# Kernel optimization log

Measured on AMD Instinct MI355X. Metric: run time of the kernel, lower is better.

## Reference

```python
import jax, jax.numpy as jnp
import numpy as np

B, S, D = 4, 2048, 512
H, KD, VD = 8, 64, 64


def glorot(key, shape):
    fan_in, fan_out = shape[-2], shape[-1]
    limit = np.sqrt(6.0 / (fan_in + fan_out)).astype(np.float32)
    return jax.random.uniform(key, shape, jnp.float32, -limit, limit)


def setup_inputs() -> dict:
    key = jax.random.key(0)
    ks = jax.random.split(key, 6)
    input_tensor = jax.random.normal(ks[0], (B, S, D), jnp.float32)
    input_mask = jnp.ones((B, S), jnp.float32)
    # Per-head projections stacked along a leading head axis [H, D, kd/vd]
    Wq = glorot(ks[1], (H, D, KD))
    Wk = glorot(ks[2], (H, D, KD))
    Wv = glorot(ks[3], (H, D, VD))
    Wo = glorot(ks[4], (H * VD, VD))
    # dot_product_scales initialized to 1 in the original (tf.Variable(1))
    scales = jnp.ones((H,), jnp.float32)
    return {"input_tensor": input_tensor, "input_mask": input_mask,
            "Wq": Wq, "Wk": Wk, "Wv": Wv, "Wo": Wo, "scales": scales}


def reference(input_tensor, input_mask, Wq, Wk, Wv, Wo, scales):
    # Vectorized over the original per-head Python loop (identical math).
    q = jnp.einsum('bsd,hdk->bhsk', input_tensor, Wq)
    k = jnp.einsum('bsd,hdk->bhsk', input_tensor, Wk)
    v = jnp.einsum('bsd,hdv->bhsv', input_tensor, Wv)
    # dotproduct notation 'bik,bjk->bij' per head, scaled by per-head scale
    scores = jnp.einsum('bhik,bhjk->bhij', q, k) * scales[None, :, None, None]
    # reshape to [..., -1] then softmax == softmax over last (key) axis here
    attn = jax.nn.softmax(scores, axis=-1)
    # kv notation 'bij,bjv,bi,bj->biv' with the mask applied twice
    ctx = jnp.einsum('bhij,bhjv,bi,bj->bhiv', attn, v, input_mask, input_mask)
    # concat heads along last axis (head-major order, as in the loop)
    ctx = jnp.transpose(ctx, (0, 2, 1, 3)).reshape(ctx.shape[0], ctx.shape[2], -1)
    return ctx @ Wo
```

## Files before the change

kernel.cpp:

```cpp
#include <hip/hip_runtime.h>
#include <hip/hip_bf16.h>


typedef _Float16 f16x8 __attribute__((ext_vector_type(8)));
typedef float    f32x4  __attribute__((ext_vector_type(4)));
typedef float    f32x16 __attribute__((ext_vector_type(16)));

#define BB 4
#define SS 2048
#define DD 512
#define HH 8
#define KDIM 64

#define EXP2F(x) __builtin_amdgcn_exp2f(x)

#define GLOAD_LDS16(gp, lp)                                                   \
  __builtin_amdgcn_global_load_lds(                                          \
      (const __attribute__((address_space(1))) void*)(gp),                    \
      (__attribute__((address_space(3))) void*)(lp), 16, 0, 0)

#define SWZ(row, bc) ((row) * 128 + ((bc) ^ (((row) & 7) << 4)))

static __device__ __forceinline__ unsigned pk2(float a, float b) {
  auto h = __builtin_amdgcn_cvt_pkrtz(a, b);
  return __builtin_bit_cast(unsigned, h);
}

union PU { unsigned u[4]; f16x8 v; };

__global__ __launch_bounds__(256) void convert_x(
    const float* __restrict__ x, _Float16* __restrict__ xf) {
  size_t i = ((size_t)blockIdx.x * 256 + threadIdx.x) * 8;
  float4 a = *(const float4*)&x[i];
  float4 b = *(const float4*)&x[i + 4];
  float vv[8] = {a.x, a.y, a.z, a.w, b.x, b.y, b.z, b.w};
  _Float16 hb[8];
#pragma unroll
  for (int u = 0; u < 8; ++u) hb[u] = (_Float16)vv[u];
  *(uint4*)&xf[i] = *(uint4*)hb;
}

__global__ __launch_bounds__(256) void convert_w(
    const float* __restrict__ Wq, const float* __restrict__ Wk,
    const float* __restrict__ Wv, _Float16* __restrict__ wtf) {
  __shared__ float s_tile[64][65];
  const int t = threadIdx.x;
  const int kb = blockIdx.x;
  const int hw = blockIdx.y;
  const int which = hw >> 3, h = hw & 7;
  const float* W = (which == 0) ? Wq : (which == 1) ? Wk : Wv;
  const float* src = W + (size_t)h * DD * KDIM + (size_t)kb * 64 * KDIM;

  {
    int kk = t >> 2, c0 = (t & 3) * 16;
#pragma unroll
    for (int u = 0; u < 4; ++u)
      *(float4*)&s_tile[kk][c0 + u * 4] = *(const float4*)&src[kk * KDIM + c0 + u * 4];
  }
  __syncthreads();

  int kd = t >> 2, kk0 = (t & 3) * 16;
  int n = which * 512 + h * 64 + kd;
  _Float16 hb[16];
#pragma unroll
  for (int u = 0; u < 16; ++u) hb[u] = (_Float16)s_tile[kk0 + u][kd];
  size_t off = (size_t)n * DD + kb * 64 + kk0;
  *(uint4*)&wtf[off] = *(uint4*)&hb[0];
  *(uint4*)&wtf[off + 8] = *(uint4*)&hb[8];
}

__global__ __launch_bounds__(256) void convert_wo(
    const float* __restrict__ Wo, _Float16* __restrict__ woT) {
  __shared__ float s_tile[64][65];
  const int t = threadIdx.x;
  const int kb = blockIdx.x;
  const float* src = Wo + (size_t)kb * 64 * 64;
  {
    int kk = t >> 2, c0 = (t & 3) * 16;
#pragma unroll
    for (int u = 0; u < 4; ++u)
      *(float4*)&s_tile[kk][c0 + u * 4] = *(const float4*)&src[kk * 64 + c0 + u * 4];
  }
  __syncthreads();
  int col = t >> 2, kk0 = (t & 3) * 16;
  _Float16 hb[16];
#pragma unroll
  for (int u = 0; u < 16; ++u) hb[u] = (_Float16)s_tile[kk0 + u][col];
  size_t off = (size_t)col * DD + kb * 64 + kk0;
  *(uint4*)&woT[off] = *(uint4*)&hb[0];
  *(uint4*)&woT[off + 8] = *(uint4*)&hb[8];
}

__global__ __launch_bounds__(256) void qkv_gemm(
    const _Float16* __restrict__ xf, const _Float16* __restrict__ wtf,
    const float* __restrict__ mask, const float* __restrict__ scales,
    _Float16* __restrict__ qf, _Float16* __restrict__ kf,
    _Float16* __restrict__ vT) {
  __shared__ _Float16 Af[128 * 32], Bf[128 * 32];
  const int t = threadIdx.x, l = t & 63, w = t >> 6;
  const int wr = w >> 1, wc = w & 1;
  const int m0 = blockIdx.y * 128, n0 = blockIdx.x * 128;

  f32x4 acc[4][4];
#pragma unroll
  for (int m = 0; m < 4; ++m)
#pragma unroll
    for (int n = 0; n < 4; ++n) acc[m][n] = f32x4{0.f, 0.f, 0.f, 0.f};

  const int rl = l >> 2, ce = (l & 3) * 8;

  for (int kt = 0; kt < 16; ++kt) {
    const int k0 = kt * 32;
    __syncthreads();
#pragma unroll
    for (int i = 0; i < 2; ++i) {
      const int row = w * 32 + i * 16;
      const size_t aoff = (size_t)(m0 + row + rl) * DD + k0 + ce;
      const size_t boff = (size_t)(n0 + row + rl) * DD + k0 + ce;
      GLOAD_LDS16(xf + aoff, &Af[row * 32]);
      GLOAD_LDS16(wtf + boff, &Bf[row * 32]);
    }
    __syncthreads();

    f16x8 ah[4], bh[4];
#pragma unroll
    for (int m = 0; m < 4; ++m) {
      int r = wr * 64 + m * 16 + (l & 15);
      ah[m] = *(const f16x8*)&Af[r * 32 + (l >> 4) * 8];
    }
#pragma unroll
    for (int n = 0; n < 4; ++n) {
      int r = wc * 64 + n * 16 + (l & 15);
      bh[n] = *(const f16x8*)&Bf[r * 32 + (l >> 4) * 8];
    }
#pragma unroll
    for (int m = 0; m < 4; ++m)
#pragma unroll
      for (int n = 0; n < 4; ++n)
        acc[m][n] = __builtin_amdgcn_mfma_f32_16x16x32_f16(ah[m], bh[n], acc[m][n], 0, 0, 0);
  }

#pragma unroll
  for (int n = 0; n < 4; ++n) {
    int colg = n0 + wc * 64 + n * 16 + (l & 15);
    int which = colg >> 9, rem = colg & 511;
    int h = rem >> 6, kd = rem & 63;
    float qsc = (which == 0) ? scales[h] * 1.44269504f : 1.f;
#pragma unroll
    for (int m = 0; m < 4; ++m) {
      int row0 = m0 + wr * 64 + m * 16 + (l >> 4) * 4;
      if (which == 2) {
        int b = row0 >> 11, s0 = row0 & 2047;
        _Float16 tmp[4] __attribute__((aligned(8)));
#pragma unroll
        for (int j = 0; j < 4; ++j)
          tmp[j] = (_Float16)(acc[m][n][j] * mask[row0 + j]);
        *(uint2*)&vT[((size_t)(b * HH + h) * KDIM + kd) * SS + s0] = *(uint2*)tmp;
      } else {
        _Float16* dst = (which == 0) ? qf : kf;
#pragma unroll
        for (int j = 0; j < 4; ++j) {
          int row = row0 + j;
          int b = row >> 11, s = row & 2047;
          dst[(((size_t)b * HH + h) * SS + s) * KDIM + kd] =
              (_Float16)(acc[m][n][j] * qsc);
        }
      }
    }
  }
}

__global__ __launch_bounds__(256) void attn_kernel(
    const _Float16* __restrict__ qg, const _Float16* __restrict__ kg,
    const _Float16* __restrict__ vTg, const float* __restrict__ mask,
    _Float16* __restrict__ ctxf) {
  const int t = threadIdx.x;
  const int l = t & 63, w = t >> 6;
  const int lr = l & 31, hi = l >> 5;
  const int bh = blockIdx.y, b = bh >> 3, h = bh & 7;
  const int q0 = blockIdx.x * 128;

  __shared__ _Float16 ksf[64 * 64];
  __shared__ _Float16 vts[64 * 64];

  const size_t base = (size_t)bh * SS * KDIM;
  const size_t vbase = (size_t)bh * KDIM * SS;

  f16x8 qfr[4];
  const int s_q = q0 + w * 32 + lr;
#pragma unroll
  for (int kb = 0; kb < 4; ++kb)
    qfr[kb] = *(const f16x8*)&qg[base + (size_t)s_q * KDIM + kb * 16 + hi * 8];

  float m_s = -1e30f, lsum = 0.f;
  f32x16 oacc[2] = {};

  for (int kt = 0; kt < SS / 64; ++kt) {
    __syncthreads();
#pragma unroll
    for (int c = 0; c < 2; ++c) {
      const int r = w * 16 + c * 8 + (l >> 3);
      const int ecol = ((l & 7) * 8) ^ (((l >> 3) & 7) * 8);
      size_t koff = base + (size_t)(kt * 64 + r) * KDIM + ecol;
      size_t voff = vbase + (size_t)r * SS + kt * 64 + ecol;
      GLOAD_LDS16(kg + koff, ksf + (w * 16 + c * 8) * 64);
      GLOAD_LDS16(vTg + voff, vts + (w * 16 + c * 8) * 64);
    }
    __syncthreads();

    f32x16 st2[2];
#pragma unroll
    for (int jb = 0; jb < 2; ++jb) {
      f32x16 acc = {};
      const int krow = jb * 32 + lr;
#pragma unroll
      for (int kb = 0; kb < 4; ++kb) {
        f16x8 kfr = *(const f16x8*)((const char*)ksf + SWZ(krow, kb * 32 + hi * 16));
        acc = __builtin_amdgcn_mfma_f32_32x32x16_f16(kfr, qfr[kb], acc, 0, 0, 0);
      }
      st2[jb] = acc;
    }

    float mt = -1e30f;
#pragma unroll
    for (int jb = 0; jb < 2; ++jb)
#pragma unroll
      for (int rr = 0; rr < 16; ++rr) mt = fmaxf(mt, st2[jb][rr]);
    mt = fmaxf(mt, __shfl_xor(mt, 32, 64));

    if (!__all(mt <= m_s + 11.5f)) {
      float mn = fmaxf(m_s, mt);
      float rs = EXP2F(m_s - mn);
      m_s = mn;
      lsum *= rs;
#pragma unroll
      for (int nb = 0; nb < 2; ++nb)
#pragma unroll
        for (int rr = 0; rr < 16; ++rr) oacc[nb][rr] *= rs;
    }

    float psum = 0.f;
    unsigned wds[2][4][2];
#pragma unroll
    for (int jb = 0; jb < 2; ++jb)
#pragma unroll
      for (int g = 0; g < 4; ++g) {
        float p0 = EXP2F(st2[jb][g * 4 + 0] - m_s);
        float p1 = EXP2F(st2[jb][g * 4 + 1] - m_s);
        float p2 = EXP2F(st2[jb][g * 4 + 2] - m_s);
        float p3 = EXP2F(st2[jb][g * 4 + 3] - m_s);
        psum += (p0 + p1) + (p2 + p3);
        wds[jb][g][0] = pk2(p0, p1);
        wds[jb][g][1] = pk2(p2, p3);
      }
    psum += __shfl_xor(psum, 32, 64);
    lsum += psum;

#pragma unroll
    for (int kb = 0; kb < 4; ++kb) {
      const int jb = kb >> 1, gb = (kb & 1) * 2;
      unsigned ow0 = hi ? wds[jb][gb + 1][0] : wds[jb][gb][0];
      unsigned ow1 = hi ? wds[jb][gb + 1][1] : wds[jb][gb][1];
      unsigned sw0 = hi ? wds[jb][gb][0] : wds[jb][gb + 1][0];
      unsigned sw1 = hi ? wds[jb][gb][1] : wds[jb][gb + 1][1];
      unsigned r0 = (unsigned)__shfl_xor((int)sw0, 32, 64);
      unsigned r1 = (unsigned)__shfl_xor((int)sw1, 32, 64);
      PU pu;
      pu.u[0] = hi ? r0 : ow0;
      pu.u[1] = hi ? r1 : ow1;
      pu.u[2] = hi ? ow0 : r0;
      pu.u[3] = hi ? ow1 : r1;
#pragma unroll
      for (int nb = 0; nb < 2; ++nb) {
        f16x8 vf = *(const f16x8*)((const char*)vts + SWZ(nb * 32 + lr, kb * 32 + hi * 16));
        oacc[nb] = __builtin_amdgcn_mfma_f32_32x32x16_f16(vf, pu.v, oacc[nb], 0, 0, 0);
      }
    }
  }

  const float inv = mask[b * SS + s_q] / lsum;
  _Float16* dst = ctxf + ((size_t)b * SS + s_q) * (HH * KDIM) + h * KDIM;
#pragma unroll
  for (int nb = 0; nb < 2; ++nb)
#pragma unroll
    for (int g = 0; g < 4; ++g) {
      uint2 o;
      o.x = pk2(oacc[nb][g * 4 + 0] * inv, oacc[nb][g * 4 + 1] * inv);
      o.y = pk2(oacc[nb][g * 4 + 2] * inv, oacc[nb][g * 4 + 3] * inv);
      *(uint2*)&dst[nb * 32 + g * 8 + hi * 4] = o;
    }
}

__global__ __launch_bounds__(256) void oproj_gemm(
    const _Float16* __restrict__ ctxf, const _Float16* __restrict__ woT,
    float* __restrict__ out) {
  __shared__ _Float16 Af[64 * 32], Bf[64 * 32];
  const int t = threadIdx.x, l = t & 63, w = t >> 6;
  const int lr = l & 31, hi = l >> 5;
  const int wr = w >> 1, wc = w & 1;
  const size_t rowbase = (size_t)blockIdx.x * 64;
  const int rl = l >> 2, ce = (l & 3) * 8;

  f32x16 acc = {};
  for (int kt = 0; kt < 16; ++kt) {
    const int k0 = kt * 32;
    __syncthreads();
    {
      const int row = w * 16;
      GLOAD_LDS16(ctxf + (rowbase + row + rl) * DD + k0 + ce, &Af[row * 32]);
      GLOAD_LDS16(woT + (size_t)(row + rl) * DD + k0 + ce, &Bf[row * 32]);
    }
    __syncthreads();
#pragma unroll
    for (int ks = 0; ks < 2; ++ks) {
      f16x8 af = *(const f16x8*)&Af[(wr * 32 + lr) * 32 + ks * 16 + hi * 8];
      f16x8 bf = *(const f16x8*)&Bf[(wc * 32 + lr) * 32 + ks * 16 + hi * 8];
      acc = __builtin_amdgcn_mfma_f32_32x32x16_f16(af, bf, acc, 0, 0, 0);
    }
  }
#pragma unroll
  for (int rr = 0; rr < 16; ++rr) {
    int m = (rr & 3) + 8 * (rr >> 2) + 4 * hi;
    out[(rowbase + wr * 32 + m) * 64 + wc * 32 + lr] = acc[rr];
  }
}

extern "C" void kernel_launch(void* const* d_in, const int* in_sizes, int n_in,
                              void* d_out, int out_size, void* d_ws, size_t ws_size,
                              hipStream_t stream) {
  const float* x     = (const float*)d_in[0];
  const float* mask  = (const float*)d_in[1];
  const float* Wq    = (const float*)d_in[2];
  const float* Wk    = (const float*)d_in[3];
  const float* Wv    = (const float*)d_in[4];
  const float* Wo    = (const float*)d_in[5];
  const float* scales= (const float*)d_in[6];
  float* out = (float*)d_out;

  char* ws = (char*)d_ws;
  const size_t xb = (size_t)BB * SS * DD * sizeof(_Float16);
  const size_t wb = (size_t)3 * 512 * DD * sizeof(_Float16);
  const size_t wob = (size_t)64 * DD * sizeof(_Float16);
  const size_t qb = (size_t)BB * HH * SS * KDIM * sizeof(_Float16);

  _Float16* xfb = (_Float16*)(ws);
  _Float16* wtfb = (_Float16*)(ws + xb);
  _Float16* woTb = (_Float16*)(ws + xb + wb);
  char* p = ws + xb + wb + wob;
  _Float16* qfb = (_Float16*)(p);
  _Float16* kfb = (_Float16*)(p + qb);
  _Float16* vTb = (_Float16*)(p + 2 * qb);
  _Float16* ctxf = (_Float16*)(p + 3 * qb);

  convert_x<<<2048, 256, 0, stream>>>(x, xfb);
  convert_w<<<dim3(8, 24), 256, 0, stream>>>(Wq, Wk, Wv, wtfb);
  convert_wo<<<8, 256, 0, stream>>>(Wo, woTb);
  qkv_gemm<<<dim3(12, 64), 256, 0, stream>>>(xfb, wtfb, mask, scales,
                                             qfb, kfb, vTb);
  attn_kernel<<<dim3(SS / 128, BB * HH), 256, 0, stream>>>(qfb, kfb, vTb, mask, ctxf);
  oproj_gemm<<<128, 256, 0, stream>>>(ctxf, woTb, out);
}
```

Baseline: 115.2 us.

## Split attention over key dimension with a log-sum-exp combine kernel

Splits the attention key loop into four chunks across a new grid dimension. Each block writes a normalized partial output in fp16 plus its log-sum-exp, and a new combine kernel merges the partials and applies the mask. This raises the block count from 512 to 2048 to fill the GPU's CUs, at the cost of extra partial-output traffic, fp16 rounding of the partials, and one more launch. It also tree-reduces the row max, sums probabilities with fdot2 on the packed fp16 values, and simplifies the lane-swap selects.

```diff
diff --git a/kernel.cpp b/kernel.cpp
--- a/kernel.cpp
+++ b/kernel.cpp
@@ -5,12 +5,15 @@
 typedef _Float16 f16x8 __attribute__((ext_vector_type(8)));
 typedef float    f32x4  __attribute__((ext_vector_type(4)));
 typedef float    f32x16 __attribute__((ext_vector_type(16)));
+typedef __fp16   hf2 __attribute__((ext_vector_type(2)));
 
 #define BB 4
 #define SS 2048
 #define DD 512
 #define HH 8
 #define KDIM 64
+#define NSPLIT 4
+#define TPS 8
 
 #define EXP2F(x) __builtin_amdgcn_exp2f(x)
 
@@ -172,13 +175,14 @@
 
 __global__ __launch_bounds__(256) void attn_kernel(
     const _Float16* __restrict__ qg, const _Float16* __restrict__ kg,
-    const _Float16* __restrict__ vTg, const float* __restrict__ mask,
-    _Float16* __restrict__ ctxf) {
+    const _Float16* __restrict__ vTg,
+    _Float16* __restrict__ po, float* __restrict__ pli) {
   const int t = threadIdx.x;
   const int l = t & 63, w = t >> 6;
   const int lr = l & 31, hi = l >> 5;
-  const int bh = blockIdx.y, b = bh >> 3, h = bh & 7;
+  const int bh = blockIdx.y;
   const int q0 = blockIdx.x * 128;
+  const int split = blockIdx.z;
 
   __shared__ _Float16 ksf[64 * 64];
   __shared__ _Float16 vts[64 * 64];
@@ -195,7 +199,8 @@
   float m_s = -1e30f, lsum = 0.f;
   f32x16 oacc[2] = {};
 
-  for (int kt = 0; kt < SS / 64; ++kt) {
+  const int kt0 = split * TPS;
+  for (int kt = kt0; kt < kt0 + TPS; ++kt) {
     __syncthreads();
 #pragma unroll
     for (int c = 0; c < 2; ++c) {
@@ -221,11 +226,14 @@
       st2[jb] = acc;
     }
 
-    float mt = -1e30f;
-#pragma unroll
-    for (int jb = 0; jb < 2; ++jb)
-#pragma unroll
-      for (int rr = 0; rr < 16; ++rr) mt = fmaxf(mt, st2[jb][rr]);
+    float m8[8];
+#pragma unroll
+    for (int i = 0; i < 8; ++i)
+      m8[i] = fmaxf(fmaxf(st2[0][i], st2[0][i + 8]),
+                    fmaxf(st2[1][i], st2[1][i + 8]));
+    float m4a = fmaxf(m8[0], m8[1]), m4b = fmaxf(m8[2], m8[3]);
+    float m4c = fmaxf(m8[4], m8[5]), m4d = fmaxf(m8[6], m8[7]);
+    float mt = fmaxf(fmaxf(m4a, m4b), fmaxf(m4c, m4d));
     mt = fmaxf(mt, __shfl_xor(mt, 32, 64));
 
     if (!__all(mt <= m_s + 11.5f)) {
@@ -239,7 +247,7 @@
         for (int rr = 0; rr < 16; ++rr) oacc[nb][rr] *= rs;
     }
 
-    float psum = 0.f;
+    float ps0 = 0.f, ps1 = 0.f;
     unsigned wds[2][4][2];
 #pragma unroll
     for (int jb = 0; jb < 2; ++jb)
@@ -249,27 +257,34 @@
         float p1 = EXP2F(st2[jb][g * 4 + 1] - m_s);
         float p2 = EXP2F(st2[jb][g * 4 + 2] - m_s);
         float p3 = EXP2F(st2[jb][g * 4 + 3] - m_s);
-        psum += (p0 + p1) + (p2 + p3);
-        wds[jb][g][0] = pk2(p0, p1);
-        wds[jb][g][1] = pk2(p2, p3);
+        unsigned pa = pk2(p0, p1), pb = pk2(p2, p3);
+        wds[jb][g][0] = pa;
+        wds[jb][g][1] = pb;
+#if __has_builtin(__builtin_amdgcn_fdot2)
+        hf2 one2 = {(__fp16)1.f, (__fp16)1.f};
+        ps0 = __builtin_amdgcn_fdot2(__builtin_bit_cast(hf2, pa), one2, ps0, false);
+        ps1 = __builtin_amdgcn_fdot2(__builtin_bit_cast(hf2, pb), one2, ps1, false);
+#else
+        ps0 += p0 + p1;
+        ps1 += p2 + p3;
+#endif
       }
+    float psum = ps0 + ps1;
     psum += __shfl_xor(psum, 32, 64);
     lsum += psum;
 
 #pragma unroll
     for (int kb = 0; kb < 4; ++kb) {
       const int jb = kb >> 1, gb = (kb & 1) * 2;
-      unsigned ow0 = hi ? wds[jb][gb + 1][0] : wds[jb][gb][0];
-      unsigned ow1 = hi ? wds[jb][gb + 1][1] : wds[jb][gb][1];
-      unsigned sw0 = hi ? wds[jb][gb][0] : wds[jb][gb + 1][0];
-      unsigned sw1 = hi ? wds[jb][gb][1] : wds[jb][gb + 1][1];
-      unsigned r0 = (unsigned)__shfl_xor((int)sw0, 32, 64);
-      unsigned r1 = (unsigned)__shfl_xor((int)sw1, 32, 64);
+      unsigned s0 = hi ? wds[jb][gb][0] : wds[jb][gb + 1][0];
+      unsigned s1 = hi ? wds[jb][gb][1] : wds[jb][gb + 1][1];
+      unsigned r0 = (unsigned)__shfl_xor((int)s0, 32, 64);
+      unsigned r1 = (unsigned)__shfl_xor((int)s1, 32, 64);
       PU pu;
-      pu.u[0] = hi ? r0 : ow0;
-      pu.u[1] = hi ? r1 : ow1;
-      pu.u[2] = hi ? ow0 : r0;
-      pu.u[3] = hi ? ow1 : r1;
+      pu.u[0] = hi ? r0 : wds[jb][gb][0];
+      pu.u[1] = hi ? r1 : wds[jb][gb][1];
+      pu.u[2] = hi ? wds[jb][gb + 1][0] : r0;
+      pu.u[3] = hi ? wds[jb][gb + 1][1] : r1;
 #pragma unroll
       for (int nb = 0; nb < 2; ++nb) {
         f16x8 vf = *(const f16x8*)((const char*)vts + SWZ(nb * 32 + lr, kb * 32 + hi * 16));
@@ -278,8 +293,9 @@
     }
   }
 
-  const float inv = mask[b * SS + s_q] / lsum;
-  _Float16* dst = ctxf + ((size_t)b * SS + s_q) * (HH * KDIM) + h * KDIM;
+  const float inv = 1.0f / lsum;
+  const float li = m_s + __log2f(lsum);
+  _Float16* prow = po + (((size_t)split * (BB * HH) + bh) * SS + s_q) * KDIM;
 #pragma unroll
   for (int nb = 0; nb < 2; ++nb)
 #pragma unroll
@@ -287,8 +303,44 @@
       uint2 o;
       o.x = pk2(oacc[nb][g * 4 + 0] * inv, oacc[nb][g * 4 + 1] * inv);
       o.y = pk2(oacc[nb][g * 4 + 2] * inv, oacc[nb][g * 4 + 3] * inv);
-      *(uint2*)&dst[nb * 32 + g * 8 + hi * 4] = o;
-    }
+      *(uint2*)&prow[nb * 32 + g * 8 + hi * 4] = o;
+    }
+  if (hi == 0)
+    pli[((size_t)split * (BB * HH) + bh) * SS + s_q] = li;
+}
+
+__global__ __launch_bounds__(256) void attn_combine(
+    const _Float16* __restrict__ po, const float* __restrict__ pli,
+    const float* __restrict__ mask, _Float16* __restrict__ ctxf) {
+  const int t = threadIdx.x;
+  const int row = blockIdx.x * 32 + (t >> 3);
+  const int c = t & 7;
+  const int bh = row >> 11, qrow = row & 2047;
+  const int b = bh >> 3, h = bh & 7;
+  const int NR = BB * HH * SS;
+
+  float li[NSPLIT];
+#pragma unroll
+  for (int s = 0; s < NSPLIT; ++s) li[s] = pli[(size_t)s * NR + row];
+  float L = fmaxf(fmaxf(li[0], li[1]), fmaxf(li[2], li[3]));
+  float wgt[NSPLIT], wsum = 0.f;
+#pragma unroll
+  for (int s = 0; s < NSPLIT; ++s) { wgt[s] = EXP2F(li[s] - L); wsum += wgt[s]; }
+
+  float acc[8] = {};
+#pragma unroll
+  for (int s = 0; s < NSPLIT; ++s) {
+    uint4 u = *(const uint4*)&po[((size_t)s * NR + row) * KDIM + c * 8];
+    const _Float16* hp = (const _Float16*)&u;
+#pragma unroll
+    for (int j = 0; j < 8; ++j) acc[j] += wgt[s] * (float)hp[j];
+  }
+  const float sc = mask[b * SS + qrow] / wsum;
+  _Float16 ob[8] __attribute__((aligned(16)));
+#pragma unroll
+  for (int j = 0; j < 8; ++j) ob[j] = (_Float16)(acc[j] * sc);
+  *(uint4*)&ctxf[((size_t)b * SS + qrow) * (HH * KDIM) + h * KDIM + c * 8] =
+      *(uint4*)ob;
 }
 
 __global__ __launch_bounds__(256) void oproj_gemm(
@@ -338,25 +390,32 @@
   float* out = (float*)d_out;
 
   char* ws = (char*)d_ws;
-  const size_t xb = (size_t)BB * SS * DD * sizeof(_Float16);
-  const size_t wb = (size_t)3 * 512 * DD * sizeof(_Float16);
+  const size_t xb  = (size_t)BB * SS * DD * sizeof(_Float16);
+  const size_t wb  = (size_t)3 * 512 * DD * sizeof(_Float16);
   const size_t wob = (size_t)64 * DD * sizeof(_Float16);
-  const size_t qb = (size_t)BB * HH * SS * KDIM * sizeof(_Float16);
-
-  _Float16* xfb = (_Float16*)(ws);
+  const size_t qb  = (size_t)BB * HH * SS * KDIM * sizeof(_Float16);
+  const size_t pob = (size_t)NSPLIT * BB * HH * SS * KDIM * sizeof(_Float16);
+  const size_t plib= (size_t)NSPLIT * BB * HH * SS * sizeof(float);
+
+  _Float16* xfb  = (_Float16*)(ws);
   _Float16* wtfb = (_Float16*)(ws + xb);
   _Float16* woTb = (_Float16*)(ws + xb + wb);
   char* p = ws + xb + wb + wob;
-  _Float16* qfb = (_Float16*)(p);
-  _Float16* kfb = (_Float16*)(p + qb);
-  _Float16* vTb = (_Float16*)(p + 2 * qb);
+  _Float16* qfb  = (_Float16*)(p);
+  _Float16* kfb  = (_Float16*)(p + qb);
+  _Float16* vTb  = (_Float16*)(p + 2 * qb);
   _Float16* ctxf = (_Float16*)(p + 3 * qb);
+  _Float16* pob_p= (_Float16*)(p + 4 * qb);
+  float*    pli_p= (float*)(p + 4 * qb + pob);
+  (void)plib; (void)ws_size;
 
   convert_x<<<2048, 256, 0, stream>>>(x, xfb);
   convert_w<<<dim3(8, 24), 256, 0, stream>>>(Wq, Wk, Wv, wtfb);
   convert_wo<<<8, 256, 0, stream>>>(Wo, woTb);
   qkv_gemm<<<dim3(12, 64), 256, 0, stream>>>(xfb, wtfb, mask, scales,
                                              qfb, kfb, vTb);
-  attn_kernel<<<dim3(SS / 128, BB * HH), 256, 0, stream>>>(qfb, kfb, vTb, mask, ctxf);
+  attn_kernel<<<dim3(SS / 128, BB * HH, NSPLIT), 256, 0, stream>>>(
+      qfb, kfb, vTb, pob_p, pli_p);
+  attn_combine<<<(BB * HH * SS) / 32, 256, 0, stream>>>(pob_p, pli_p, mask, ctxf);
   oproj_gemm<<<128, 256, 0, stream>>>(ctxf, woTb, out);
 }
```

Measured after the change: 121.2 us. 1.05x slower.

## Fuse fp32-to-fp16 input conversion into QKV GEMM and prioritize attention MFMAs

Applied to the files above, without the earlier changes.

Removes the separate convert_x kernel. The QKV GEMM now loads fp32 x tiles straight into swizzled LDS and packs them to fp16 when reading fragments, which drops a full-tensor round trip through the workspace and one kernel launch. The attention loop also raises wave priority around the MFMA sections, reduces the row max as a tree, and splits the partial sum into two accumulators to add ILP. In exchange, each QKV block moves twice as many bytes for A into LDS, and the fp32 x tile is re-read by all 12 column blocks instead of being converted once.

```diff
diff --git a/kernel.cpp b/kernel.cpp
--- a/kernel.cpp
+++ b/kernel.cpp
@@ -27,18 +27,6 @@
 }
 
 union PU { unsigned u[4]; f16x8 v; };
-
-__global__ __launch_bounds__(256) void convert_x(
-    const float* __restrict__ x, _Float16* __restrict__ xf) {
-  size_t i = ((size_t)blockIdx.x * 256 + threadIdx.x) * 8;
-  float4 a = *(const float4*)&x[i];
-  float4 b = *(const float4*)&x[i + 4];
-  float vv[8] = {a.x, a.y, a.z, a.w, b.x, b.y, b.z, b.w};
-  _Float16 hb[8];
-#pragma unroll
-  for (int u = 0; u < 8; ++u) hb[u] = (_Float16)vv[u];
-  *(uint4*)&xf[i] = *(uint4*)hb;
-}
 
 __global__ __launch_bounds__(256) void convert_w(
     const float* __restrict__ Wq, const float* __restrict__ Wk,
@@ -92,11 +80,12 @@
 }
 
 __global__ __launch_bounds__(256) void qkv_gemm(
-    const _Float16* __restrict__ xf, const _Float16* __restrict__ wtf,
+    const float* __restrict__ x, const _Float16* __restrict__ wtf,
     const float* __restrict__ mask, const float* __restrict__ scales,
     _Float16* __restrict__ qf, _Float16* __restrict__ kf,
     _Float16* __restrict__ vT) {
-  __shared__ _Float16 Af[128 * 32], Bf[128 * 32];
+  __shared__ float    Af32[128 * 32];
+  __shared__ _Float16 Bf[128 * 32];
   const int t = threadIdx.x, l = t & 63, w = t >> 6;
   const int wr = w >> 1, wc = w & 1;
   const int m0 = blockIdx.y * 128, n0 = blockIdx.x * 128;
@@ -107,18 +96,24 @@
 #pragma unroll
     for (int n = 0; n < 4; ++n) acc[m][n] = f32x4{0.f, 0.f, 0.f, 0.f};
 
-  const int rl = l >> 2, ce = (l & 3) * 8;
+  const int rlb = l >> 2, ceb = (l & 3) * 8;
+  const int rla = l >> 3;
+  const int swa = (((l & 7) * 16) ^ ((rla & 7) << 4)) >> 2;
 
   for (int kt = 0; kt < 16; ++kt) {
     const int k0 = kt * 32;
     __syncthreads();
 #pragma unroll
+    for (int c = 0; c < 4; ++c) {
+      const int rowg = w * 32 + c * 8;
+      GLOAD_LDS16(x + (size_t)(m0 + rowg + rla) * DD + k0 + swa,
+                  &Af32[rowg * 32]);
+    }
+#pragma unroll
     for (int i = 0; i < 2; ++i) {
-      const int row = w * 32 + i * 16;
-      const size_t aoff = (size_t)(m0 + row + rl) * DD + k0 + ce;
-      const size_t boff = (size_t)(n0 + row + rl) * DD + k0 + ce;
-      GLOAD_LDS16(xf + aoff, &Af[row * 32]);
-      GLOAD_LDS16(wtf + boff, &Bf[row * 32]);
+      const int rowg = w * 32 + i * 16;
+      GLOAD_LDS16(wtf + (size_t)(n0 + rowg + rlb) * DD + k0 + ceb,
+                  &Bf[rowg * 32]);
     }
     __syncthreads();
 
@@ -126,7 +121,15 @@
 #pragma unroll
     for (int m = 0; m < 4; ++m) {
       int r = wr * 64 + m * 16 + (l & 15);
-      ah[m] = *(const f16x8*)&Af[r * 32 + (l >> 4) * 8];
+      int cb = (l >> 4) * 32;
+      float4 fa = *(const float4*)((const char*)Af32 + r * 128 + ((cb) ^ ((r & 7) << 4)));
+      float4 fb = *(const float4*)((const char*)Af32 + r * 128 + ((cb + 16) ^ ((r & 7) << 4)));
+      PU pu;
+      pu.u[0] = pk2(fa.x, fa.y);
+      pu.u[1] = pk2(fa.z, fa.w);
+      pu.u[2] = pk2(fb.x, fb.y);
+      pu.u[3] = pk2(fb.z, fb.w);
+      ah[m] = pu.v;
     }
 #pragma unroll
     for (int n = 0; n < 4; ++n) {
@@ -209,6 +212,7 @@
     __syncthreads();
 
     f32x16 st2[2];
+    __builtin_amdgcn_s_setprio(1);
 #pragma unroll
     for (int jb = 0; jb < 2; ++jb) {
       f32x16 acc = {};
@@ -220,12 +224,16 @@
       }
       st2[jb] = acc;
     }
-
-    float mt = -1e30f;
-#pragma unroll
-    for (int jb = 0; jb < 2; ++jb)
-#pragma unroll
-      for (int rr = 0; rr < 16; ++rr) mt = fmaxf(mt, st2[jb][rr]);
+    __builtin_amdgcn_s_setprio(0);
+
+    float m8[8];
+#pragma unroll
+    for (int i = 0; i < 8; ++i)
+      m8[i] = fmaxf(fmaxf(st2[0][i], st2[0][i + 8]),
+                    fmaxf(st2[1][i], st2[1][i + 8]));
+    float m4a = fmaxf(m8[0], m8[1]), m4b = fmaxf(m8[2], m8[3]);
+    float m4c = fmaxf(m8[4], m8[5]), m4d = fmaxf(m8[6], m8[7]);
+    float mt = fmaxf(fmaxf(m4a, m4b), fmaxf(m4c, m4d));
     mt = fmaxf(mt, __shfl_xor(mt, 32, 64));
 
     if (!__all(mt <= m_s + 11.5f)) {
@@ -239,7 +247,7 @@
         for (int rr = 0; rr < 16; ++rr) oacc[nb][rr] *= rs;
     }
 
-    float psum = 0.f;
+    float ps0 = 0.f, ps1 = 0.f;
     unsigned wds[2][4][2];
 #pragma unroll
     for (int jb = 0; jb < 2; ++jb)
@@ -249,32 +257,34 @@
         float p1 = EXP2F(st2[jb][g * 4 + 1] - m_s);
         float p2 = EXP2F(st2[jb][g * 4 + 2] - m_s);
         float p3 = EXP2F(st2[jb][g * 4 + 3] - m_s);
-        psum += (p0 + p1) + (p2 + p3);
+        ps0 += p0 + p1;
+        ps1 += p2 + p3;
         wds[jb][g][0] = pk2(p0, p1);
         wds[jb][g][1] = pk2(p2, p3);
       }
+    float psum = ps0 + ps1;
     psum += __shfl_xor(psum, 32, 64);
     lsum += psum;
 
 #pragma unroll
     for (int kb = 0; kb < 4; ++kb) {
       const int jb = kb >> 1, gb = (kb & 1) * 2;
-      unsigned ow0 = hi ? wds[jb][gb + 1][0] : wds[jb][gb][0];
-      unsigned ow1 = hi ? wds[jb][gb + 1][1] : wds[jb][gb][1];
-      unsigned sw0 = hi ? wds[jb][gb][0] : wds[jb][gb + 1][0];
-      unsigned sw1 = hi ? wds[jb][gb][1] : wds[jb][gb + 1][1];
-      unsigned r0 = (unsigned)__shfl_xor((int)sw0, 32, 64);
-      unsigned r1 = (unsigned)__shfl_xor((int)sw1, 32, 64);
+      unsigned s0 = hi ? wds[jb][gb][0] : wds[jb][gb + 1][0];
+      unsigned s1 = hi ? wds[jb][gb][1] : wds[jb][gb + 1][1];
+      unsigned r0 = (unsigned)__shfl_xor((int)s0, 32, 64);
+      unsigned r1 = (unsigned)__shfl_xor((int)s1, 32, 64);
       PU pu;
-      pu.u[0] = hi ? r0 : ow0;
-      pu.u[1] = hi ? r1 : ow1;
-      pu.u[2] = hi ? ow0 : r0;
-      pu.u[3] = hi ? ow1 : r1;
+      pu.u[0] = hi ? r0 : wds[jb][gb][0];
+      pu.u[1] = hi ? r1 : wds[jb][gb][1];
+      pu.u[2] = hi ? wds[jb][gb + 1][0] : r0;
+      pu.u[3] = hi ? wds[jb][gb + 1][1] : r1;
+      __builtin_amdgcn_s_setprio(1);
 #pragma unroll
       for (int nb = 0; nb < 2; ++nb) {
         f16x8 vf = *(const f16x8*)((const char*)vts + SWZ(nb * 32 + lr, kb * 32 + hi * 16));
         oacc[nb] = __builtin_amdgcn_mfma_f32_32x32x16_f16(vf, pu.v, oacc[nb], 0, 0, 0);
       }
+      __builtin_amdgcn_s_setprio(0);
     }
   }
 
@@ -338,24 +348,22 @@
   float* out = (float*)d_out;
 
   char* ws = (char*)d_ws;
-  const size_t xb = (size_t)BB * SS * DD * sizeof(_Float16);
-  const size_t wb = (size_t)3 * 512 * DD * sizeof(_Float16);
+  const size_t wb  = (size_t)3 * 512 * DD * sizeof(_Float16);
   const size_t wob = (size_t)64 * DD * sizeof(_Float16);
-  const size_t qb = (size_t)BB * HH * SS * KDIM * sizeof(_Float16);
-
-  _Float16* xfb = (_Float16*)(ws);
-  _Float16* wtfb = (_Float16*)(ws + xb);
-  _Float16* woTb = (_Float16*)(ws + xb + wb);
-  char* p = ws + xb + wb + wob;
-  _Float16* qfb = (_Float16*)(p);
-  _Float16* kfb = (_Float16*)(p + qb);
-  _Float16* vTb = (_Float16*)(p + 2 * qb);
+  const size_t qb  = (size_t)BB * HH * SS * KDIM * sizeof(_Float16);
+
+  _Float16* wtfb = (_Float16*)(ws);
+  _Float16* woTb = (_Float16*)(ws + wb);
+  char* p = ws + wb + wob;
+  _Float16* qfb  = (_Float16*)(p);
+  _Float16* kfb  = (_Float16*)(p + qb);
+  _Float16* vTb  = (_Float16*)(p + 2 * qb);
   _Float16* ctxf = (_Float16*)(p + 3 * qb);
-
-  convert_x<<<2048, 256, 0, stream>>>(x, xfb);
+  (void)ws_size;
+
   convert_w<<<dim3(8, 24), 256, 0, stream>>>(Wq, Wk, Wv, wtfb);
   convert_wo<<<8, 256, 0, stream>>>(Wo, woTb);
-  qkv_gemm<<<dim3(12, 64), 256, 0, stream>>>(xfb, wtfb, mask, scales,
+  qkv_gemm<<<dim3(12, 64), 256, 0, stream>>>(x, wtfb, mask, scales,
                                              qfb, kfb, vTb);
   attn_kernel<<<dim3(SS / 128, BB * HH), 256, 0, stream>>>(qfb, kfb, vTb, mask, ctxf);
   oproj_gemm<<<128, 256, 0, stream>>>(ctxf, woTb, out);
```

After: 121.5 us. +5.5%, slower.
